# Performance work log

Measured on AMD Instinct MI355X. Metric: run time of the kernel, lower is better.

## Reference

```python
import jax, jax.numpy as jnp
import numpy as np

N, L, D = 256, 512, 512


def _attention(x, W_in, W_out, apply_tanh):
    # x: [N, L, D]; 'general' attention: project query, score against context (=x)
    q = jnp.einsum('bld,ed->ble', x, W_in)          # [N, L, D]
    scores = jnp.einsum('bld,bmd->blm', q, x)       # [N, L, L]
    w = jax.nn.softmax(scores, axis=-1)             # softmax over keys
    mix = jnp.einsum('blm,bmd->bld', w, x)          # [N, L, D]
    comb = jnp.concatenate([mix, q], axis=-1)       # [N, L, 2D]
    out = jnp.einsum('blc,dc->bld', comb, W_out)    # Linear(2D, D), no bias
    return jnp.tanh(out) if apply_tanh else out


def setup_inputs() -> dict:
    key = jax.random.key(0)
    k1, k2, k3, k4, k5 = jax.random.split(key, 5)
    s = 0.02
    return {
        'embeddings': jax.random.normal(k1, (N, L, D), dtype=jnp.float32),
        'W_in1': jax.random.normal(k2, (D, D), dtype=jnp.float32) * s,
        'W_out1': jax.random.normal(k3, (D, 2 * D), dtype=jnp.float32) * s,
        'W_in2': jax.random.normal(k4, (D, D), dtype=jnp.float32) * s,
        'W_out2': jax.random.normal(k5, (D, 2 * D), dtype=jnp.float32) * s,
    }


def reference(embeddings, W_in1, W_out1, W_in2, W_out2):
    x = _attention(embeddings, W_in1, W_out1, apply_tanh=True)   # block 1 (tanh)
    x = _attention(x, W_in2, W_out2, apply_tanh=False)           # block 2 (no tanh)
    # transpose(1,2) + avg_pool1d over full length == mean over L
    pooled = jnp.mean(x, axis=1)                                  # [N, D]
    return pooled.reshape(pooled.shape[0], -1, 1, 1)              # [N, D, 1, 1]
```

## Files before the change

### kernel.cpp

```cpp
#include <hip/hip_runtime.h>
#include <cstdint>
#include <cstddef>

typedef uint16_t u16;
typedef __attribute__((ext_vector_type(8))) short bf16x8;
typedef __attribute__((ext_vector_type(4))) float f32x4;
typedef __attribute__((ext_vector_type(4))) uint16_t u16x4;

#define GLOBAL_AS(p) (const __attribute__((address_space(1))) void*)(p)
#define LDS_AS(p)    (__attribute__((address_space(3))) void*)(p)

__device__ __forceinline__ u16 f2b(float f){
  uint32_t u = __float_as_uint(f);
  u += 0x7fff + ((u >> 16) & 1);
  return (u16)(u >> 16);
}
__device__ __forceinline__ float b2f(u16 h){
  return __uint_as_float(((uint32_t)h) << 16);
}

__global__ void cvt_bf16_kernel(const float* __restrict__ src, u16* __restrict__ dst, int n){
  int i = (blockIdx.x * 256 + threadIdx.x) * 4;
  if (i >= n) return;
  float4 f = *(const float4*)(src + i);
  u16x4 o; o.x = f2b(f.x); o.y = f2b(f.y); o.z = f2b(f.z); o.w = f2b(f.w);
  *(u16x4*)(dst + i) = o;
}

__global__ void transpose512_kernel(const u16* __restrict__ src, u16* __restrict__ dst){
  __shared__ u16 tile[64][68];
  size_t b = blockIdx.y;
  int t = blockIdx.x;
  int r0 = (t >> 3) * 64, c0 = (t & 7) * 64;
  const u16* s = src + b * 262144;
  u16* d = dst + b * 262144;
  int tx = threadIdx.x & 63, ty = threadIdx.x >> 6;
  #pragma unroll
  for (int k = 0; k < 16; k++){
    int r = ty * 16 + k;
    tile[r][tx] = s[(size_t)(r0 + r) * 512 + c0 + tx];
  }
  __syncthreads();
  #pragma unroll
  for (int k = 0; k < 16; k++){
    int c = ty * 16 + k;
    d[(size_t)(c0 + c) * 512 + r0 + tx] = tile[tx][c];
  }
}

__global__ void softmax_kernel(const float* __restrict__ S, u16* __restrict__ P){
  int row = blockIdx.x * 4 + (threadIdx.x >> 6);
  int lane = threadIdx.x & 63;
  const float* s = S + (size_t)row * 512;
  float v[8];
  float mx = -3.0e38f;
  #pragma unroll
  for (int i = 0; i < 8; i++){ v[i] = s[lane + i * 64]; mx = fmaxf(mx, v[i]); }
  #pragma unroll
  for (int o = 32; o > 0; o >>= 1) mx = fmaxf(mx, __shfl_xor(mx, o));
  float sum = 0.f;
  #pragma unroll
  for (int i = 0; i < 8; i++){ v[i] = __expf(v[i] - mx); sum += v[i]; }
  #pragma unroll
  for (int o = 32; o > 0; o >>= 1) sum += __shfl_xor(sum, o);
  float inv = 1.0f / sum;
  u16* p = P + (size_t)row * 512;
  #pragma unroll
  for (int i = 0; i < 8; i++) p[lane + i * 64] = f2b(v[i] * inv);
}

__global__ void pool_kernel(const u16* __restrict__ O, float* __restrict__ out, int b0){
  size_t b = blockIdx.x;
  int t = threadIdx.x;
  const u16* p = O + b * 262144;
  float s0 = 0.f, s1 = 0.f;
  for (int l = 0; l < 512; l++){
    s0 += b2f(p[l * 512 + t]);
    s1 += b2f(p[l * 512 + t + 256]);
  }
  float* o = out + ((size_t)b0 + b) * 512;
  o[t]       = s0 * (1.0f / 512.0f);
  o[t + 256] = s1 * (1.0f / 512.0f);
}

template<bool SPLIT, bool TANH, typename CT>
__global__ __launch_bounds__(256, 2) void gemm_bt_kernel(
    const u16* __restrict__ A0, const u16* __restrict__ A1,
    const u16* __restrict__ B, CT* __restrict__ C,
    int K, int ldb, int64_t aBatch, int64_t bBatch, int64_t cBatch)
{
  __shared__ __align__(16) u16 As[128 * 32];
  __shared__ __align__(16) u16 Bs[128 * 32];
  int64_t bat = blockIdx.y;
  int m0 = (blockIdx.x >> 2) * 128, n0 = (blockIdx.x & 3) * 128;
  A0 += bat * aBatch;
  if (SPLIT) A1 += bat * aBatch;
  B += bat * bBatch;
  C += bat * cBatch;
  int tid = threadIdx.x, lane = tid & 63;
  int w = tid >> 6;
  int wm = (w >> 1) * 64, wn = (w & 1) * 64;
  f32x4 acc[4][4];
  #pragma unroll
  for (int i = 0; i < 4; i++)
    #pragma unroll
    for (int j = 0; j < 4; j++) acc[i][j] = (f32x4){0.f, 0.f, 0.f, 0.f};

  int sRow = tid >> 2, sCol = (tid & 3) * 8;
  int fr = lane & 15, fq = (lane >> 4) * 8;

  for (int k0 = 0; k0 < K; k0 += 32){
    const u16* Ap = A0; int kk = k0;
    if (SPLIT && k0 >= 512){ Ap = A1; kk = k0 - 512; }
    const u16* ga = Ap + (size_t)(m0 + sRow) * 512 + kk + sCol;
    const u16* gb = B  + (size_t)(n0 + sRow) * ldb + k0 + sCol;
    __builtin_amdgcn_global_load_lds(GLOBAL_AS(ga),                    LDS_AS(&As[tid * 8]),        16, 0, 0);
    __builtin_amdgcn_global_load_lds(GLOBAL_AS(ga + (size_t)64 * 512), LDS_AS(&As[2048 + tid * 8]), 16, 0, 0);
    __builtin_amdgcn_global_load_lds(GLOBAL_AS(gb),                    LDS_AS(&Bs[tid * 8]),        16, 0, 0);
    __builtin_amdgcn_global_load_lds(GLOBAL_AS(gb + (size_t)64 * ldb), LDS_AS(&Bs[2048 + tid * 8]), 16, 0, 0);
    __syncthreads();
    bf16x8 af[4], bfr[4];
    #pragma unroll
    for (int i = 0; i < 4; i++) af[i]  = *(const bf16x8*)&As[(wm + i * 16 + fr) * 32 + fq];
    #pragma unroll
    for (int j = 0; j < 4; j++) bfr[j] = *(const bf16x8*)&Bs[(wn + j * 16 + fr) * 32 + fq];
    #pragma unroll
    for (int i = 0; i < 4; i++)
      #pragma unroll
      for (int j = 0; j < 4; j++)
        acc[i][j] = __builtin_amdgcn_mfma_f32_16x16x32_bf16(af[i], bfr[j], acc[i][j], 0, 0, 0);
    __syncthreads();
  }
  int cq = (lane >> 4) * 4, cc = lane & 15;
  #pragma unroll
  for (int i = 0; i < 4; i++){
    #pragma unroll
    for (int j = 0; j < 4; j++){
      #pragma unroll
      for (int r = 0; r < 4; r++){
        int row = m0 + wm + i * 16 + cq + r;
        int col = n0 + wn + j * 16 + cc;
        float v = acc[i][j][r];
        if (TANH) v = tanhf(v);
        if constexpr (sizeof(CT) == 4) C[(size_t)row * 512 + col] = v;
        else                           C[(size_t)row * 512 + col] = f2b(v);
      }
    }
  }
}

extern "C" void kernel_launch(void* const* d_in, const int* in_sizes, int n_in,
                              void* d_out, int out_size, void* d_ws, size_t ws_size,
                              hipStream_t stream) {
  const float* emb   = (const float*)d_in[0];
  const float* Win1  = (const float*)d_in[1];
  const float* Wout1 = (const float*)d_in[2];
  const float* Win2  = (const float*)d_in[3];
  const float* Wout2 = (const float*)d_in[4];
  float* out = (float*)d_out;

  int CB = 64;
  while (CB > 1 && (4ull << 20) + (size_t)CB * (262144ull * 16) > ws_size) CB >>= 1;
  const int64_t S = (int64_t)CB * 262144;

  char* wsb = (char*)d_ws;
  u16* Win1b  = (u16*)wsb;
  u16* Wout1b = Win1b + 262144;
  u16* Win2b  = Wout1b + 524288;
  u16* Wout2b = Win2b + 262144;
  u16* base = (u16*)(wsb + (4 << 20));
  u16* xb   = base;
  u16* x2b  = xb + S;
  u16* qb   = x2b + S;
  u16* mixb = qb + S;
  u16* xTb  = mixb + S;
  float* scb = (float*)(xTb + S);
  u16* Pb   = (u16*)(scb + S);
  u16* out2b = (u16*)scb;

  cvt_bf16_kernel<<<256, 256, 0, stream>>>(Win1,  Win1b,  262144);
  cvt_bf16_kernel<<<512, 256, 0, stream>>>(Wout1, Wout1b, 524288);
  cvt_bf16_kernel<<<256, 256, 0, stream>>>(Win2,  Win2b,  262144);
  cvt_bf16_kernel<<<512, 256, 0, stream>>>(Wout2, Wout2b, 524288);

  dim3 gg(16, CB);
  dim3 gt(64, CB);
  const int64_t s1 = 262144;

  for (int c = 0; c < 256 / CB; c++){
    const float* embc = emb + (size_t)c * CB * 262144;
    cvt_bf16_kernel<<<CB * 256, 256, 0, stream>>>(embc, xb, CB * 262144);

    gemm_bt_kernel<false,false,u16><<<gg, 256, 0, stream>>>(xb, nullptr, Win1b, qb, 512, 512, s1, 0, s1);
    transpose512_kernel<<<gt, 256, 0, stream>>>(xb, xTb);
    gemm_bt_kernel<false,false,float><<<gg, 256, 0, stream>>>(qb, nullptr, xb, scb, 512, 512, s1, s1, s1);
    softmax_kernel<<<CB * 128, 256, 0, stream>>>(scb, Pb);
    gemm_bt_kernel<false,false,u16><<<gg, 256, 0, stream>>>(Pb, nullptr, xTb, mixb, 512, 512, s1, s1, s1);
    gemm_bt_kernel<true,true,u16><<<gg, 256, 0, stream>>>(mixb, qb, Wout1b, x2b, 1024, 1024, s1, 0, s1);

    gemm_bt_kernel<false,false,u16><<<gg, 256, 0, stream>>>(x2b, nullptr, Win2b, qb, 512, 512, s1, 0, s1);
    transpose512_kernel<<<gt, 256, 0, stream>>>(x2b, xTb);
    gemm_bt_kernel<false,false,float><<<gg, 256, 0, stream>>>(qb, nullptr, x2b, scb, 512, 512, s1, s1, s1);
    softmax_kernel<<<CB * 128, 256, 0, stream>>>(scb, Pb);
    gemm_bt_kernel<false,false,u16><<<gg, 256, 0, stream>>>(Pb, nullptr, xTb, mixb, 512, 512, s1, s1, s1);
    gemm_bt_kernel<true,false,u16><<<gg, 256, 0, stream>>>(mixb, qb, Wout2b, out2b, 1024, 1024, s1, 0, s1);

    pool_kernel<<<CB, 256, 0, stream>>>(out2b, out, c * CB);
  }
}
```

Measured before the change: 1.994 ms.

## Fuse pooling into final GEMM epilogue, fuse convert+transpose, shrink workspace

The final output GEMM now reduces its tile over rows and atomically adds the mean into the pooled output, so the full block-2 output is never written and the separate pool kernel goes away. The fp32-to-bf16 embedding conversion is fused with the first transpose. Workspace buffers are reused across stages, cutting per-batch memory so the chunk size can grow to all 256 batches and fewer launches are needed. Atomic accumulation adds nondeterministic summation order and requires a memset of the output.

```diff
diff --git a/kernel.cpp b/kernel.cpp
--- a/kernel.cpp
+++ b/kernel.cpp
@@ -25,6 +25,30 @@
   float4 f = *(const float4*)(src + i);
   u16x4 o; o.x = f2b(f.x); o.y = f2b(f.y); o.z = f2b(f.z); o.w = f2b(f.w);
   *(u16x4*)(dst + i) = o;
+}
+
+__global__ void cvtT_kernel(const float* __restrict__ src, u16* __restrict__ x, u16* __restrict__ xT){
+  __shared__ u16 tile[64][68];
+  size_t b = blockIdx.y;
+  int t = blockIdx.x;
+  int r0 = (t >> 3) * 64, c0 = (t & 7) * 64;
+  const float* s = src + b * 262144;
+  u16* dx = x + b * 262144;
+  u16* dT = xT + b * 262144;
+  int tx = threadIdx.x & 63, ty = threadIdx.x >> 6;
+  #pragma unroll
+  for (int k = 0; k < 16; k++){
+    int r = ty * 16 + k;
+    u16 v = f2b(s[(size_t)(r0 + r) * 512 + c0 + tx]);
+    dx[(size_t)(r0 + r) * 512 + c0 + tx] = v;
+    tile[r][tx] = v;
+  }
+  __syncthreads();
+  #pragma unroll
+  for (int k = 0; k < 16; k++){
+    int c = ty * 16 + k;
+    dT[(size_t)(c0 + c) * 512 + r0 + tx] = tile[tx][c];
+  }
 }
 
 __global__ void transpose512_kernel(const u16* __restrict__ src, u16* __restrict__ dst){
@@ -69,25 +93,12 @@
   for (int i = 0; i < 8; i++) p[lane + i * 64] = f2b(v[i] * inv);
 }
 
-__global__ void pool_kernel(const u16* __restrict__ O, float* __restrict__ out, int b0){
-  size_t b = blockIdx.x;
-  int t = threadIdx.x;
-  const u16* p = O + b * 262144;
-  float s0 = 0.f, s1 = 0.f;
-  for (int l = 0; l < 512; l++){
-    s0 += b2f(p[l * 512 + t]);
-    s1 += b2f(p[l * 512 + t + 256]);
-  }
-  float* o = out + ((size_t)b0 + b) * 512;
-  o[t]       = s0 * (1.0f / 512.0f);
-  o[t + 256] = s1 * (1.0f / 512.0f);
-}
-
-template<bool SPLIT, bool TANH, typename CT>
+template<bool SPLIT, bool TANH, bool POOL, typename CT>
 __global__ __launch_bounds__(256, 2) void gemm_bt_kernel(
     const u16* __restrict__ A0, const u16* __restrict__ A1,
     const u16* __restrict__ B, CT* __restrict__ C,
-    int K, int ldb, int64_t aBatch, int64_t bBatch, int64_t cBatch)
+    int K, int ldb, int64_t aBatch, int64_t bBatch, int64_t cBatch,
+    float* __restrict__ poolOut, int b0)
 {
   __shared__ __align__(16) u16 As[128 * 32];
   __shared__ __align__(16) u16 Bs[128 * 32];
@@ -96,7 +107,7 @@
   A0 += bat * aBatch;
   if (SPLIT) A1 += bat * aBatch;
   B += bat * bBatch;
-  C += bat * cBatch;
+  if (!POOL) C += bat * cBatch;
   int tid = threadIdx.x, lane = tid & 63;
   int w = tid >> 6;
   int wm = (w >> 1) * 64, wn = (w & 1) * 64;
@@ -131,19 +142,37 @@
         acc[i][j] = __builtin_amdgcn_mfma_f32_16x16x32_bf16(af[i], bfr[j], acc[i][j], 0, 0, 0);
     __syncthreads();
   }
-  int cq = (lane >> 4) * 4, cc = lane & 15;
-  #pragma unroll
-  for (int i = 0; i < 4; i++){
+
+  if constexpr (POOL){
     #pragma unroll
     for (int j = 0; j < 4; j++){
+      float p = 0.f;
       #pragma unroll
-      for (int r = 0; r < 4; r++){
-        int row = m0 + wm + i * 16 + cq + r;
-        int col = n0 + wn + j * 16 + cc;
-        float v = acc[i][j][r];
-        if (TANH) v = tanhf(v);
-        if constexpr (sizeof(CT) == 4) C[(size_t)row * 512 + col] = v;
-        else                           C[(size_t)row * 512 + col] = f2b(v);
+      for (int i = 0; i < 4; i++)
+        #pragma unroll
+        for (int r = 0; r < 4; r++) p += acc[i][j][r];
+      p += __shfl_xor(p, 16);
+      p += __shfl_xor(p, 32);
+      if (lane < 16){
+        int col = n0 + wn + j * 16 + lane;
+        atomicAdd(poolOut + ((size_t)(b0) + bat) * 512 + col, p * (1.0f / 512.0f));
+      }
+    }
+  } else {
+    int cq = (lane >> 4) * 4, cc = lane & 15;
+    #pragma unroll
+    for (int i = 0; i < 4; i++){
+      #pragma unroll
+      for (int j = 0; j < 4; j++){
+        #pragma unroll
+        for (int r = 0; r < 4; r++){
+          int row = m0 + wm + i * 16 + cq + r;
+          int col = n0 + wn + j * 16 + cc;
+          float v = acc[i][j][r];
+          if (TANH) v = tanhf(v);
+          if constexpr (sizeof(CT) == 4) C[(size_t)row * 512 + col] = v;
+          else                           C[(size_t)row * 512 + col] = f2b(v);
+        }
       }
     }
   }
@@ -159,9 +188,9 @@
   const float* Wout2 = (const float*)d_in[4];
   float* out = (float*)d_out;
 
-  int CB = 64;
-  while (CB > 1 && (4ull << 20) + (size_t)CB * (262144ull * 16) > ws_size) CB >>= 1;
-  const int64_t S = (int64_t)CB * 262144;
+  int CB = 256;
+  while (CB > 1 && (4ull << 20) + (size_t)CB * (3ull << 20) > ws_size) CB >>= 1;
+  const int64_t E = 262144;
 
   char* wsb = (char*)d_ws;
   u16* Win1b  = (u16*)wsb;
@@ -169,14 +198,13 @@
   u16* Win2b  = Wout1b + 524288;
   u16* Wout2b = Win2b + 262144;
   u16* base = (u16*)(wsb + (4 << 20));
-  u16* xb   = base;
-  u16* x2b  = xb + S;
-  u16* qb   = x2b + S;
-  u16* mixb = qb + S;
-  u16* xTb  = mixb + S;
-  float* scb = (float*)(xTb + S);
-  u16* Pb   = (u16*)(scb + S);
-  u16* out2b = (u16*)scb;
+  u16*   Ar  = base;
+  u16*   Br  = base + (size_t)CB * E;
+  u16*   Cr  = base + 2 * (size_t)CB * E;
+  float* Dr  = (float*)(base + 3 * (size_t)CB * E);
+  u16*   Fr  = base + 5 * (size_t)CB * E;
+
+  hipMemsetAsync(d_out, 0, (size_t)out_size * sizeof(float), stream);
 
   cvt_bf16_kernel<<<256, 256, 0, stream>>>(Win1,  Win1b,  262144);
   cvt_bf16_kernel<<<512, 256, 0, stream>>>(Wout1, Wout1b, 524288);
@@ -185,26 +213,31 @@
 
   dim3 gg(16, CB);
   dim3 gt(64, CB);
-  const int64_t s1 = 262144;
 
   for (int c = 0; c < 256 / CB; c++){
     const float* embc = emb + (size_t)c * CB * 262144;
-    cvt_bf16_kernel<<<CB * 256, 256, 0, stream>>>(embc, xb, CB * 262144);
-
-    gemm_bt_kernel<false,false,u16><<<gg, 256, 0, stream>>>(xb, nullptr, Win1b, qb, 512, 512, s1, 0, s1);
-    transpose512_kernel<<<gt, 256, 0, stream>>>(xb, xTb);
-    gemm_bt_kernel<false,false,float><<<gg, 256, 0, stream>>>(qb, nullptr, xb, scb, 512, 512, s1, s1, s1);
-    softmax_kernel<<<CB * 128, 256, 0, stream>>>(scb, Pb);
-    gemm_bt_kernel<false,false,u16><<<gg, 256, 0, stream>>>(Pb, nullptr, xTb, mixb, 512, 512, s1, s1, s1);
-    gemm_bt_kernel<true,true,u16><<<gg, 256, 0, stream>>>(mixb, qb, Wout1b, x2b, 1024, 1024, s1, 0, s1);
-
-    gemm_bt_kernel<false,false,u16><<<gg, 256, 0, stream>>>(x2b, nullptr, Win2b, qb, 512, 512, s1, 0, s1);
-    transpose512_kernel<<<gt, 256, 0, stream>>>(x2b, xTb);
-    gemm_bt_kernel<false,false,float><<<gg, 256, 0, stream>>>(qb, nullptr, x2b, scb, 512, 512, s1, s1, s1);
-    softmax_kernel<<<CB * 128, 256, 0, stream>>>(scb, Pb);
-    gemm_bt_kernel<false,false,u16><<<gg, 256, 0, stream>>>(Pb, nullptr, xTb, mixb, 512, 512, s1, s1, s1);
-    gemm_bt_kernel<true,false,u16><<<gg, 256, 0, stream>>>(mixb, qb, Wout2b, out2b, 1024, 1024, s1, 0, s1);
-
-    pool_kernel<<<CB, 256, 0, stream>>>(out2b, out, c * CB);
-  }
-}
+    int b0 = c * CB;
+
+    cvtT_kernel<<<gt, 256, 0, stream>>>(embc, Ar, Cr);
+    gemm_bt_kernel<false,false,false,u16><<<gg, 256, 0, stream>>>(
+        Ar, nullptr, Win1b, Br, 512, 512, E, 0, E, nullptr, 0);
+    gemm_bt_kernel<false,false,false,float><<<gg, 256, 0, stream>>>(
+        Br, nullptr, Ar, Dr, 512, 512, E, E, 262144, nullptr, 0);
+    softmax_kernel<<<CB * 128, 256, 0, stream>>>(Dr, Fr);
+    gemm_bt_kernel<false,false,false,u16><<<gg, 256, 0, stream>>>(
+        Fr, nullptr, Cr, Ar, 512, 512, E, E, E, nullptr, 0);
+    gemm_bt_kernel<true,true,false,u16><<<gg, 256, 0, stream>>>(
+        Ar, Br, Wout1b, Cr, 1024, 1024, E, 0, E, nullptr, 0);
+
+    gemm_bt_kernel<false,false,false,u16><<<gg, 256, 0, stream>>>(
+        Cr, nullptr, Win2b, Br, 512, 512, E, 0, E, nullptr, 0);
+    transpose512_kernel<<<gt, 256, 0, stream>>>(Cr, Fr);
+    gemm_bt_kernel<false,false,false,float><<<gg, 256, 0, stream>>>(
+        Br, nullptr, Cr, Dr, 512, 512, E, E, 262144, nullptr, 0);
+    softmax_kernel<<<CB * 128, 256, 0, stream>>>(Dr, Ar);
+    gemm_bt_kernel<false,false,false,u16><<<gg, 256, 0, stream>>>(
+        Ar, nullptr, Fr, Cr, 512, 512, E, E, E, nullptr, 0);
+    gemm_bt_kernel<true,false,true,u16><<<gg, 256, 0, stream>>>(
+        Cr, Br, Wout2b, (u16*)nullptr, 1024, 1024, E, 0, 0, out, b0);
+  }
+}
```

New measurement: 1.887 ms. 1.06x faster.
